# Performance work log

Hardware: AMD Instinct MI355X
Metric: run time of the kernel (lower is better)

Reference implementation:

```python
import jax, jax.numpy as jnp
import numpy as np

B, W, H, C = 8, 32, 32, 64   # batch, width, height, hidden_size
NH = 8                        # num_attention_heads
M = 32                        # max_position_embeddings
P = C // 2                    # position_embedding_size (query_positional_score=True)


def setup_inputs() -> dict:
    key = jax.random.key(0)
    ks = jax.random.split(key, 7)
    s = 0.02
    return {
        "hidden_states": jax.random.normal(ks[0], (B, W, H, C), dtype=jnp.float32),
        "row_emb": jax.random.normal(ks[1], (2 * M - 1, P), dtype=jnp.float32) * s,
        "col_emb": jax.random.normal(ks[2], (2 * M - 1, P), dtype=jnp.float32) * s,
        "Wq": jax.random.normal(ks[3], (NH * C, C), dtype=jnp.float32) * s,
        "bq": jnp.zeros((NH * C,), dtype=jnp.float32),
        "Wk": jax.random.normal(ks[4], (NH * C, C), dtype=jnp.float32) * s,
        "bk": jnp.zeros((NH * C,), dtype=jnp.float32),
        "Wv": jax.random.normal(ks[5], (C, NH * C), dtype=jnp.float32) * s,
        "bv": jnp.zeros((C,), dtype=jnp.float32),
    }


def reference(hidden_states, row_emb, col_emb, Wq, bq, Wk, bk, Wv, bv):
    b, w, h, c = hidden_states.shape
    nh = Wq.shape[0] // c
    half = c // 2
    center = row_emb.shape[0] // 2  # = max_position_embeddings - 1

    # projections: all_head_size = nh * c (per source: hidden_size * num_heads)
    q = (hidden_states @ Wq.T + bq).reshape(b, w, h, nh, c)
    k = (hidden_states @ Wk.T + bk).reshape(b, w, h, nh, c)

    # relative index tables: rel[i, j] = (j - i) + (M - 1)
    iw = jnp.arange(w)
    ih = jnp.arange(h)
    rel_w = iw[None, :] - iw[:, None] + center   # (w, w)
    rel_h = ih[None, :] - ih[:, None] + center   # (h, h)
    r_emb = row_emb[rel_w]  # (w, w, P)
    c_emb = col_emb[rel_h]  # (h, h, P)

    # positional scores: q split into row/col halves
    q_row = q[..., :half]
    q_col = q[..., half:]
    row_scores = jnp.einsum('bijhd,ikd->bijhk', q_row, r_emb)  # (b,w,h,nh,w)
    col_scores = jnp.einsum('bijhd,jld->bijhl', q_col, c_emb)  # (b,w,h,nh,h)
    scale = jnp.sqrt(jnp.asarray(c, dtype=hidden_states.dtype))
    scores = (row_scores[..., :, None] + col_scores[..., None, :]) / scale  # (b,w,h,nh,w,h)

    # content scores q^T k
    scores = scores + jnp.einsum('bijhd,bklhd->bijhkl', q, k) / scale

    # softmax over merged spatial key dims (k,l)
    probs = jax.nn.softmax(scores.reshape(b, w, h, nh, w * h), axis=-1).reshape(scores.shape)

    # value mixing directly with hidden_states, then output projection
    mixed = jnp.einsum('bijhkl,bkld->bijhd', probs, hidden_states).reshape(b, w, h, nh * c)
    return mixed @ Wv.T + bv
```

## Files before the change

kernel.cpp:

```cpp
#include <hip/hip_runtime.h>
#include <math.h>

typedef __bf16 bf16;
typedef bf16 bf16x2 __attribute__((ext_vector_type(2)));
typedef bf16 bf16x4 __attribute__((ext_vector_type(4)));
typedef bf16 bf16x8 __attribute__((ext_vector_type(8)));
typedef float f32x4 __attribute__((ext_vector_type(4)));

constexpr int CENTER = 31;

static __device__ __forceinline__ unsigned short f2bf_bits(float f) {
    bf16 b = (bf16)f;
    return __builtin_bit_cast(unsigned short, b);
}

__global__ __launch_bounds__(256)
void qkproj_kernel(const float* __restrict__ hid,
                   const float* __restrict__ Wq, const float* __restrict__ bq,
                   const float* __restrict__ Wk, const float* __restrict__ bk,
                   bf16* __restrict__ qb, bf16* __restrict__ kb,
                   bf16* __restrict__ htb)
{
    __shared__ __attribute__((aligned(16))) bf16 As[128][72];
    __shared__ __attribute__((aligned(16))) bf16 Bs[128][72];

    const int t  = threadIdx.x;
    const int pt = blockIdx.x;
    const int ot = blockIdx.y;
    const int z  = blockIdx.z;
    const float* W    = z ? Wk : Wq;
    const float* bias = z ? bk : bq;
    bf16* outp        = z ? kb : qb;
    const float scale = z ? 1.0f : 0.125f;
    const int p0 = pt * 128;
    const int b  = p0 >> 10;

    {
        int row = t >> 1, ch = (t & 1) * 32;
        const float4* asrc = (const float4*)(hid + (size_t)(p0 + row) * 64 + ch);
        const float4* bsrc = (const float4*)(W + (size_t)(ot * 128 + row) * 64 + ch);
        bf16 ta[32], tb[32];
        #pragma unroll
        for (int u = 0; u < 8; ++u) {
            float4 va = asrc[u], vb = bsrc[u];
            ta[4*u+0] = (bf16)va.x; ta[4*u+1] = (bf16)va.y;
            ta[4*u+2] = (bf16)va.z; ta[4*u+3] = (bf16)va.w;
            tb[4*u+0] = (bf16)vb.x; tb[4*u+1] = (bf16)vb.y;
            tb[4*u+2] = (bf16)vb.z; tb[4*u+3] = (bf16)vb.w;
        }
        #pragma unroll
        for (int u = 0; u < 4; ++u) {
            *(int4*)&As[row][ch + u * 8] = ((int4*)ta)[u];
            *(int4*)&Bs[row][ch + u * 8] = ((int4*)tb)[u];
        }
    }
    __syncthreads();

    if (ot == 0 && z == 0) {
        int d = t >> 2, ps = (t & 3) * 32;
        bf16* hdst = htb + ((size_t)b * 64 + d) * 1024 + (p0 & 1023) + ps;
        #pragma unroll
        for (int ii = 0; ii < 32; ii += 2) {
            ushort2 pk;
            pk.x = __builtin_bit_cast(unsigned short, As[ps + ii][d]);
            pk.y = __builtin_bit_cast(unsigned short, As[ps + ii + 1][d]);
            *(ushort2*)(hdst + ii) = pk;
        }
    }

    const int w = t >> 6, ln = t & 63, l15 = ln & 15, quad = ln >> 4;

    bf16x8 a[2][2];
    #pragma unroll
    for (int mt = 0; mt < 2; ++mt) {
        a[mt][0] = *(const bf16x8*)&As[w * 32 + mt * 16 + l15][quad * 8];
        a[mt][1] = *(const bf16x8*)&As[w * 32 + mt * 16 + l15][32 + quad * 8];
    }

    const f32x4 z4 = {0.f, 0.f, 0.f, 0.f};
    f32x4 acc[2][8];
    #pragma unroll
    for (int mt = 0; mt < 2; ++mt)
        #pragma unroll
        for (int nt = 0; nt < 8; ++nt) acc[mt][nt] = z4;

    #pragma unroll
    for (int nt = 0; nt < 8; ++nt) {
        bf16x8 b0 = *(const bf16x8*)&Bs[nt * 16 + l15][quad * 8];
        bf16x8 b1 = *(const bf16x8*)&Bs[nt * 16 + l15][32 + quad * 8];
        #pragma unroll
        for (int mt = 0; mt < 2; ++mt) {
            acc[mt][nt] = __builtin_amdgcn_mfma_f32_16x16x32_bf16(a[mt][0], b0, acc[mt][nt], 0, 0, 0);
            acc[mt][nt] = __builtin_amdgcn_mfma_f32_16x16x32_bf16(a[mt][1], b1, acc[mt][nt], 0, 0, 0);
        }
    }

    #pragma unroll
    for (int nt = 0; nt < 8; ++nt) {
        int o = ot * 128 + nt * 16 + l15;
        float bv = bias[o];
        int hh = o >> 6, d = o & 63;
        #pragma unroll
        for (int mt = 0; mt < 2; ++mt)
            #pragma unroll
            for (int r = 0; r < 4; ++r) {
                int pos = (p0 & 1023) + w * 32 + mt * 16 + quad * 4 + r;
                float val = (acc[mt][nt][r] + bv) * scale;
                outp[(((size_t)b * 8 + hh) * 1024 + pos) * 64 + d] = (bf16)val;
            }
    }
}

__global__ __launch_bounds__(256)
void bias_kernel(const bf16* __restrict__ qb,
                 const float* __restrict__ row_emb, const float* __restrict__ col_emb,
                 bf16* __restrict__ rowbias, bf16* __restrict__ colbias)
{
    __shared__ __attribute__((aligned(16))) bf16 embRs[63][40];
    __shared__ __attribute__((aligned(16))) bf16 embCs[63][40];

    const int t  = threadIdx.x;
    const int bh = blockIdx.x;
    const int sg = blockIdx.y;

    for (int i = t; i < 2016; i += 256) embRs[i >> 5][i & 31] = (bf16)row_emb[i];
    for (int i = t; i < 2016; i += 256) embCs[i >> 5][i & 31] = (bf16)col_emb[i];
    __syncthreads();

    const int w = t >> 6, ln = t & 63, l15 = ln & 15, quad = ln >> 4;

    #pragma unroll
    for (int u = 0; u < 4; ++u) {
        int s = sg * 16 + u * 4 + w;
        bool cm = s >= 32;
        int ij = cm ? s - 32 : s;

        bf16x8 a[2];
        #pragma unroll
        for (int mt = 0; mt < 2; ++mt) {
            const bf16* ap = cm
                ? qb + ((size_t)bh * 1024 + (mt * 16 + l15) * 32 + ij) * 64 + 32 + quad * 8
                : qb + ((size_t)bh * 1024 + ij * 32 + mt * 16 + l15) * 64 + quad * 8;
            a[mt] = *(const bf16x8*)ap;
        }
        bf16* ob = cm ? colbias : rowbias;

        #pragma unroll
        for (int nt = 0; nt < 2; ++nt) {
            int erow = nt * 16 + l15 + CENTER - ij;
            bf16x8 bfrag = cm ? *(const bf16x8*)&embCs[erow][quad * 8]
                              : *(const bf16x8*)&embRs[erow][quad * 8];
            #pragma unroll
            for (int mt = 0; mt < 2; ++mt) {
                f32x4 c = {0.f, 0.f, 0.f, 0.f};
                c = __builtin_amdgcn_mfma_f32_16x16x32_bf16(a[mt], bfrag, c, 0, 0, 0);
                #pragma unroll
                for (int r = 0; r < 4; ++r) {
                    int ql = mt * 16 + quad * 4 + r;
                    int qrow = cm ? ql * 32 + ij : ij * 32 + ql;
                    ob[((size_t)bh * 1024 + qrow) * 32 + nt * 16 + l15] = (bf16)c[r];
                }
            }
        }
    }
}

__global__ __launch_bounds__(256, 2)
void attn_kernel(const bf16* __restrict__ qb, const bf16* __restrict__ kb,
                 const bf16* __restrict__ htb,
                 const bf16* __restrict__ rowbias, const bf16* __restrict__ colbias,
                 bf16* __restrict__ mixedb)
{
    __shared__ __attribute__((aligned(16))) bf16 Ks[64][72];
    __shared__ __attribute__((aligned(16))) bf16 Hts[64][72];
    __shared__ __attribute__((aligned(16))) bf16 Pp[4][32][72];

    const int t  = threadIdx.x;
    const int qt = blockIdx.x;
    const int bh = blockIdx.y;
    const int b  = bh >> 3, h = bh & 7;
    const int q0 = qt * 128;
    const int w = t >> 6, ln = t & 63, l15 = ln & 15, quad = ln >> 4;

    bf16x8 bq_[2][2];
    float  cbv[2][2][4];
    const bf16* rbp[2];
    #pragma unroll
    for (int mt = 0; mt < 2; ++mt) {
        int qrow = q0 + w * 32 + mt * 16 + l15;
        const bf16* qp = qb + ((size_t)bh * 1024 + qrow) * 64;
        bq_[mt][0] = *(const bf16x8*)(qp + quad * 8);
        bq_[mt][1] = *(const bf16x8*)(qp + 32 + quad * 8);
        #pragma unroll
        for (int par = 0; par < 2; ++par) {
            bf16x4 cv = *(const bf16x4*)(colbias + ((size_t)bh * 1024 + qrow) * 32 + par * 16 + quad * 4);
            #pragma unroll
            for (int r = 0; r < 4; ++r) cbv[mt][par][r] = (float)cv[r];
        }
        rbp[mt] = rowbias + ((size_t)bh * 1024 + qrow) * 32;
    }

    const f32x4 z4 = {0.f, 0.f, 0.f, 0.f};
    f32x4 oacc[2][4];
    float lsum[2] = {0.f, 0.f};
    #pragma unroll
    for (int mt = 0; mt < 2; ++mt)
        #pragma unroll
        for (int dt = 0; dt < 4; ++dt) oacc[mt][dt] = z4;

    bf16* Pw = &Pp[w][0][0];
    const bf16* kcbase = kb + (size_t)bh * 1024 * 64;
    const bf16* hcbase = htb + (size_t)b * 64 * 1024;

    for (int kc = 0; kc < 16; ++kc) {
        __syncthreads();
        {
            int row = t >> 2, c = (t & 3) << 4;
            const bf16* ksrc = kcbase + (size_t)(kc * 64 + row) * 64 + c;
            *(int4*)&Ks[row][c]     = *(const int4*)ksrc;
            *(int4*)&Ks[row][c + 8] = *(const int4*)(ksrc + 8);
            const bf16* hsrc = hcbase + (size_t)row * 1024 + kc * 64 + c;
            *(int4*)&Hts[row][c]     = *(const int4*)hsrc;
            *(int4*)&Hts[row][c + 8] = *(const int4*)(hsrc + 8);
        }
        float rb[2][2];
        #pragma unroll
        for (int mt = 0; mt < 2; ++mt) {
            bf16x2 rv = *(const bf16x2*)(rbp[mt] + kc * 2);
            rb[mt][0] = (float)rv[0]; rb[mt][1] = (float)rv[1];
        }
        __syncthreads();

        f32x4 sf[2][4];
        #pragma unroll
        for (int mt = 0; mt < 2; ++mt)
            #pragma unroll
            for (int kt = 0; kt < 4; ++kt) sf[mt][kt] = z4;
        #pragma unroll
        for (int kt = 0; kt < 4; ++kt) {
            bf16x8 aK0 = *(const bf16x8*)&Ks[kt * 16 + l15][quad * 8];
            bf16x8 aK1 = *(const bf16x8*)&Ks[kt * 16 + l15][32 + quad * 8];
            #pragma unroll
            for (int mt = 0; mt < 2; ++mt) {
                sf[mt][kt] = __builtin_amdgcn_mfma_f32_16x16x32_bf16(aK0, bq_[mt][0], sf[mt][kt], 0, 0, 0);
                sf[mt][kt] = __builtin_amdgcn_mfma_f32_16x16x32_bf16(aK1, bq_[mt][1], sf[mt][kt], 0, 0, 0);
            }
        }

        #pragma unroll
        for (int mt = 0; mt < 2; ++mt)
            #pragma unroll
            for (int kt = 0; kt < 4; ++kt) {
                float rbv = rb[mt][kt >> 1];
                ushort4 pk;
                float p0 = __expf(sf[mt][kt][0] + rbv + cbv[mt][kt & 1][0]);
                float p1 = __expf(sf[mt][kt][1] + rbv + cbv[mt][kt & 1][1]);
                float p2 = __expf(sf[mt][kt][2] + rbv + cbv[mt][kt & 1][2]);
                float p3 = __expf(sf[mt][kt][3] + rbv + cbv[mt][kt & 1][3]);
                lsum[mt] += (p0 + p1) + (p2 + p3);
                pk.x = f2bf_bits(p0); pk.y = f2bf_bits(p1);
                pk.z = f2bf_bits(p2); pk.w = f2bf_bits(p3);
                *(ushort4*)&Pw[(mt * 16 + l15) * 72 + kt * 16 + quad * 4] = pk;
            }

        bf16x8 bp[2][2];
        #pragma unroll
        for (int mt = 0; mt < 2; ++mt) {
            bp[mt][0] = *(const bf16x8*)&Pw[(mt * 16 + l15) * 72 + quad * 8];
            bp[mt][1] = *(const bf16x8*)&Pw[(mt * 16 + l15) * 72 + 32 + quad * 8];
        }
        #pragma unroll
        for (int dt = 0; dt < 4; ++dt) {
            bf16x8 aH0 = *(const bf16x8*)&Hts[dt * 16 + l15][quad * 8];
            bf16x8 aH1 = *(const bf16x8*)&Hts[dt * 16 + l15][32 + quad * 8];
            #pragma unroll
            for (int mt = 0; mt < 2; ++mt) {
                oacc[mt][dt] = __builtin_amdgcn_mfma_f32_16x16x32_bf16(aH0, bp[mt][0], oacc[mt][dt], 0, 0, 0);
                oacc[mt][dt] = __builtin_amdgcn_mfma_f32_16x16x32_bf16(aH1, bp[mt][1], oacc[mt][dt], 0, 0, 0);
            }
        }
    }

    float inv[2];
    #pragma unroll
    for (int mt = 0; mt < 2; ++mt) {
        float v = lsum[mt];
        v += __shfl_xor(v, 16);
        v += __shfl_xor(v, 32);
        inv[mt] = 1.0f / v;
    }
    #pragma unroll
    for (int mt = 0; mt < 2; ++mt) {
        int pos = q0 + w * 32 + mt * 16 + l15;
        bf16* mb = mixedb + ((size_t)b * 1024 + pos) * 512 + h * 64;
        #pragma unroll
        for (int dt = 0; dt < 4; ++dt) {
            ushort4 pk;
            pk.x = f2bf_bits(oacc[mt][dt][0] * inv[mt]);
            pk.y = f2bf_bits(oacc[mt][dt][1] * inv[mt]);
            pk.z = f2bf_bits(oacc[mt][dt][2] * inv[mt]);
            pk.w = f2bf_bits(oacc[mt][dt][3] * inv[mt]);
            *(ushort4*)(mb + dt * 16 + quad * 4) = pk;
        }
    }
}

__global__ __launch_bounds__(256)
void out_proj_kernel(const bf16* __restrict__ mixedb,
                     const float* __restrict__ Wv, const float* __restrict__ bv,
                     float* __restrict__ out)
{
    __shared__ __attribute__((aligned(16))) bf16 Wvs[64][264];

    const int t  = threadIdx.x;
    const int p0 = blockIdx.x * 64;
    const int w = t >> 6, ln = t & 63, l15 = ln & 15, quad = ln >> 4;

    f32x4 acc[4];
    #pragma unroll
    for (int nt = 0; nt < 4; ++nt) {
        float bvv = bv[nt * 16 + l15];
        acc[nt] = (f32x4){bvv, bvv, bvv, bvv};
    }

    const bf16* arow = mixedb + (size_t)(p0 + w * 16 + l15) * 512;

    for (int half = 0; half < 2; ++half) {
        __syncthreads();
        {
            int c = t >> 2, seg = (t & 3) * 64;
            const float4* src = (const float4*)(Wv + (size_t)c * 512 + half * 256 + seg);
            #pragma unroll
            for (int u = 0; u < 16; ++u) {
                float4 v = src[u];
                bf16x4 pk = {(bf16)v.x, (bf16)v.y, (bf16)v.z, (bf16)v.w};
                *(bf16x4*)&Wvs[c][seg + u * 4] = pk;
            }
        }
        __syncthreads();

        #pragma unroll
        for (int kc = 0; kc < 8; ++kc) {
            bf16x8 a = *(const bf16x8*)(arow + half * 256 + kc * 32 + quad * 8);
            #pragma unroll
            for (int nt = 0; nt < 4; ++nt) {
                bf16x8 bfrag = *(const bf16x8*)&Wvs[nt * 16 + l15][kc * 32 + quad * 8];
                acc[nt] = __builtin_amdgcn_mfma_f32_16x16x32_bf16(a, bfrag, acc[nt], 0, 0, 0);
            }
        }
    }

    #pragma unroll
    for (int nt = 0; nt < 4; ++nt)
        #pragma unroll
        for (int r = 0; r < 4; ++r)
            out[(size_t)(p0 + w * 16 + quad * 4 + r) * 64 + nt * 16 + l15] = acc[nt][r];
}

extern "C" void kernel_launch(void* const* d_in, const int* in_sizes, int n_in,
                              void* d_out, int out_size, void* d_ws, size_t ws_size,
                              hipStream_t stream)
{
    const float* hid     = (const float*)d_in[0];
    const float* row_emb = (const float*)d_in[1];
    const float* col_emb = (const float*)d_in[2];
    const float* Wq      = (const float*)d_in[3];
    const float* bq      = (const float*)d_in[4];
    const float* Wk      = (const float*)d_in[5];
    const float* bk      = (const float*)d_in[6];
    const float* Wv      = (const float*)d_in[7];
    const float* bv      = (const float*)d_in[8];
    float* out = (float*)d_out;

    bf16* qb  = (bf16*)d_ws;
    bf16* kb  = qb + (size_t)64 * 1024 * 64;
    bf16* htb = kb + (size_t)64 * 1024 * 64;
    bf16* rowbias = htb + (size_t)8 * 64 * 1024;
    bf16* colbias = rowbias + (size_t)64 * 1024 * 32;
    bf16* mixedb  = colbias + (size_t)64 * 1024 * 32;

    qkproj_kernel<<<dim3(64, 4, 2), 256, 0, stream>>>(hid, Wq, bq, Wk, bk, qb, kb, htb);
    bias_kernel<<<dim3(64, 4), 256, 0, stream>>>(qb, row_emb, col_emb, rowbias, colbias);
    attn_kernel<<<dim3(8, 64), 256, 0, stream>>>(qb, kb, htb, rowbias, colbias, mixedb);
    out_proj_kernel<<<128, 256, 0, stream>>>(mixedb, Wv, bv, out);
}
```

Before: 135.1 us.

## Load K and hidden-state fragments directly from global in MFMA-ready layout

```diff
diff --git a/kernel.cpp b/kernel.cpp
--- a/kernel.cpp
+++ b/kernel.cpp
@@ -19,7 +19,7 @@
                    const float* __restrict__ Wq, const float* __restrict__ bq,
                    const float* __restrict__ Wk, const float* __restrict__ bk,
                    bf16* __restrict__ qb, bf16* __restrict__ kb,
-                   bf16* __restrict__ htb)
+                   bf16* __restrict__ htp)
 {
     __shared__ __attribute__((aligned(16))) bf16 As[128][72];
     __shared__ __attribute__((aligned(16))) bf16 Bs[128][72];
@@ -58,13 +58,18 @@
 
     if (ot == 0 && z == 0) {
         int d = t >> 2, ps = (t & 3) * 32;
-        bf16* hdst = htb + ((size_t)b * 64 + d) * 1024 + (p0 & 1023) + ps;
-        #pragma unroll
-        for (int ii = 0; ii < 32; ii += 2) {
-            ushort2 pk;
-            pk.x = __builtin_bit_cast(unsigned short, As[ps + ii][d]);
+        int pp = (p0 & 1023) + ps;
+        int kc = pp >> 6, half = (pp >> 5) & 1;
+        bf16* hdst = htp + (size_t)b * 65536 + kc * 4096 + half * 2048
+                         + (d >> 4) * 512 + (d & 15) * 32;
+        #pragma unroll
+        for (int ii = 0; ii < 32; ii += 4) {
+            ushort4 pk;
+            pk.x = __builtin_bit_cast(unsigned short, As[ps + ii + 0][d]);
             pk.y = __builtin_bit_cast(unsigned short, As[ps + ii + 1][d]);
-            *(ushort2*)(hdst + ii) = pk;
+            pk.z = __builtin_bit_cast(unsigned short, As[ps + ii + 2][d]);
+            pk.w = __builtin_bit_cast(unsigned short, As[ps + ii + 3][d]);
+            *(ushort4*)(hdst + ii) = pk;
         }
     }
 
@@ -165,14 +170,12 @@
     }
 }
 
-__global__ __launch_bounds__(256, 2)
+__global__ __launch_bounds__(256, 3)
 void attn_kernel(const bf16* __restrict__ qb, const bf16* __restrict__ kb,
-                 const bf16* __restrict__ htb,
+                 const bf16* __restrict__ htp,
                  const bf16* __restrict__ rowbias, const bf16* __restrict__ colbias,
                  bf16* __restrict__ mixedb)
 {
-    __shared__ __attribute__((aligned(16))) bf16 Ks[64][72];
-    __shared__ __attribute__((aligned(16))) bf16 Hts[64][72];
     __shared__ __attribute__((aligned(16))) bf16 Pp[4][32][72];
 
     const int t  = threadIdx.x;
@@ -209,42 +212,32 @@
         for (int dt = 0; dt < 4; ++dt) oacc[mt][dt] = z4;
 
     bf16* Pw = &Pp[w][0][0];
-    const bf16* kcbase = kb + (size_t)bh * 1024 * 64;
-    const bf16* hcbase = htb + (size_t)b * 64 * 1024;
+    const bf16* kfrag = kb + (size_t)bh * 65536 + (size_t)l15 * 64 + quad * 8;
+    const bf16* hfrag = htp + (size_t)b * 65536 + (size_t)l15 * 32 + quad * 8;
 
     for (int kc = 0; kc < 16; ++kc) {
-        __syncthreads();
-        {
-            int row = t >> 2, c = (t & 3) << 4;
-            const bf16* ksrc = kcbase + (size_t)(kc * 64 + row) * 64 + c;
-            *(int4*)&Ks[row][c]     = *(const int4*)ksrc;
-            *(int4*)&Ks[row][c + 8] = *(const int4*)(ksrc + 8);
-            const bf16* hsrc = hcbase + (size_t)row * 1024 + kc * 64 + c;
-            *(int4*)&Hts[row][c]     = *(const int4*)hsrc;
-            *(int4*)&Hts[row][c + 8] = *(const int4*)(hsrc + 8);
-        }
+        f32x4 sf[2][4];
+        #pragma unroll
+        for (int mt = 0; mt < 2; ++mt)
+            #pragma unroll
+            for (int kt = 0; kt < 4; ++kt) sf[mt][kt] = z4;
+        #pragma unroll
+        for (int kt = 0; kt < 4; ++kt) {
+            const bf16* kp = kfrag + (size_t)(kc * 64 + kt * 16) * 64;
+            bf16x8 aK0 = *(const bf16x8*)kp;
+            bf16x8 aK1 = *(const bf16x8*)(kp + 32);
+            #pragma unroll
+            for (int mt = 0; mt < 2; ++mt) {
+                sf[mt][kt] = __builtin_amdgcn_mfma_f32_16x16x32_bf16(aK0, bq_[mt][0], sf[mt][kt], 0, 0, 0);
+                sf[mt][kt] = __builtin_amdgcn_mfma_f32_16x16x32_bf16(aK1, bq_[mt][1], sf[mt][kt], 0, 0, 0);
+            }
+        }
+
         float rb[2][2];
         #pragma unroll
         for (int mt = 0; mt < 2; ++mt) {
             bf16x2 rv = *(const bf16x2*)(rbp[mt] + kc * 2);
             rb[mt][0] = (float)rv[0]; rb[mt][1] = (float)rv[1];
-        }
-        __syncthreads();
-
-        f32x4 sf[2][4];
-        #pragma unroll
-        for (int mt = 0; mt < 2; ++mt)
-            #pragma unroll
-            for (int kt = 0; kt < 4; ++kt) sf[mt][kt] = z4;
-        #pragma unroll
-        for (int kt = 0; kt < 4; ++kt) {
-            bf16x8 aK0 = *(const bf16x8*)&Ks[kt * 16 + l15][quad * 8];
-            bf16x8 aK1 = *(const bf16x8*)&Ks[kt * 16 + l15][32 + quad * 8];
-            #pragma unroll
-            for (int mt = 0; mt < 2; ++mt) {
-                sf[mt][kt] = __builtin_amdgcn_mfma_f32_16x16x32_bf16(aK0, bq_[mt][0], sf[mt][kt], 0, 0, 0);
-                sf[mt][kt] = __builtin_amdgcn_mfma_f32_16x16x32_bf16(aK1, bq_[mt][1], sf[mt][kt], 0, 0, 0);
-            }
         }
 
         #pragma unroll
@@ -271,8 +264,9 @@
         }
         #pragma unroll
         for (int dt = 0; dt < 4; ++dt) {
-            bf16x8 aH0 = *(const bf16x8*)&Hts[dt * 16 + l15][quad * 8];
-            bf16x8 aH1 = *(const bf16x8*)&Hts[dt * 16 + l15][32 + quad * 8];
+            const bf16* hp = hfrag + kc * 4096 + dt * 512;
+            bf16x8 aH0 = *(const bf16x8*)hp;
+            bf16x8 aH1 = *(const bf16x8*)(hp + 2048);
             #pragma unroll
             for (int mt = 0; mt < 2; ++mt) {
                 oacc[mt][dt] = __builtin_amdgcn_mfma_f32_16x16x32_bf16(aH0, bp[mt][0], oacc[mt][dt], 0, 0, 0);
@@ -374,13 +368,13 @@
 
     bf16* qb  = (bf16*)d_ws;
     bf16* kb  = qb + (size_t)64 * 1024 * 64;
-    bf16* htb = kb + (size_t)64 * 1024 * 64;
-    bf16* rowbias = htb + (size_t)8 * 64 * 1024;
+    bf16* htp = kb + (size_t)64 * 1024 * 64;
+    bf16* rowbias = htp + (size_t)8 * 64 * 1024;
     bf16* colbias = rowbias + (size_t)64 * 1024 * 32;
     bf16* mixedb  = colbias + (size_t)64 * 1024 * 32;
 
-    qkproj_kernel<<<dim3(64, 4, 2), 256, 0, stream>>>(hid, Wq, bq, Wk, bk, qb, kb, htb);
+    qkproj_kernel<<<dim3(64, 4, 2), 256, 0, stream>>>(hid, Wq, bq, Wk, bk, qb, kb, htp);
     bias_kernel<<<dim3(64, 4), 256, 0, stream>>>(qb, row_emb, col_emb, rowbias, colbias);
-    attn_kernel<<<dim3(8, 64), 256, 0, stream>>>(qb, kb, htb, rowbias, colbias, mixedb);
+    attn_kernel<<<dim3(8, 64), 256, 0, stream>>>(qb, kb, htp, rowbias, colbias, mixedb);
     out_proj_kernel<<<128, 256, 0, stream>>>(mixedb, Wv, bv, out);
 }
```

After: 157.3 us. 1.16x slower.

## Add prep kernel converting inputs and weights to bf16 once; merge Q/K projection blocks

Applied to the files above, without the earlier changes.

```diff
diff --git a/kernel.cpp b/kernel.cpp
--- a/kernel.cpp
+++ b/kernel.cpp
@@ -15,58 +15,94 @@
 }
 
 __global__ __launch_bounds__(256)
-void qkproj_kernel(const float* __restrict__ hid,
-                   const float* __restrict__ Wq, const float* __restrict__ bq,
-                   const float* __restrict__ Wk, const float* __restrict__ bk,
-                   bf16* __restrict__ qb, bf16* __restrict__ kb,
-                   bf16* __restrict__ htb)
+void prep_kernel(const float* __restrict__ hid,
+                 const float* __restrict__ Wq, const float* __restrict__ Wk,
+                 const float* __restrict__ Wv,
+                 bf16* __restrict__ hb, bf16* __restrict__ htb,
+                 bf16* __restrict__ Wqb, bf16* __restrict__ Wkb,
+                 bf16* __restrict__ Wvb)
+{
+    __shared__ __attribute__((aligned(16))) bf16 hs[64][72];
+
+    const int t   = threadIdx.x;
+    const int blk = blockIdx.x;
+    const int b   = blk >> 4, kc = blk & 15;
+
+    {
+        int row = t >> 2, c4 = (t & 3) * 16;
+        const float4* src = (const float4*)(hid + ((size_t)b * 1024 + kc * 64 + row) * 64 + c4);
+        bf16 tmp[16];
+        #pragma unroll
+        for (int u = 0; u < 4; ++u) {
+            float4 v = src[u];
+            tmp[4*u+0] = (bf16)v.x; tmp[4*u+1] = (bf16)v.y;
+            tmp[4*u+2] = (bf16)v.z; tmp[4*u+3] = (bf16)v.w;
+        }
+        *(int4*)&hs[row][c4]     = ((int4*)tmp)[0];
+        *(int4*)&hs[row][c4 + 8] = ((int4*)tmp)[1];
+        bf16* hdst = hb + ((size_t)b * 1024 + kc * 64 + row) * 64 + c4;
+        *(int4*)hdst       = ((int4*)tmp)[0];
+        *(int4*)(hdst + 8) = ((int4*)tmp)[1];
+    }
+
+    {
+        int idx = blk * 256 + t;
+        if (idx < 8192) {
+            float4 vq = ((const float4*)Wq)[idx];
+            float4 vk = ((const float4*)Wk)[idx];
+            float4 vv = ((const float4*)Wv)[idx];
+            ushort4 pq, pk2, pv;
+            pq.x = f2bf_bits(vq.x); pq.y = f2bf_bits(vq.y); pq.z = f2bf_bits(vq.z); pq.w = f2bf_bits(vq.w);
+            pk2.x = f2bf_bits(vk.x); pk2.y = f2bf_bits(vk.y); pk2.z = f2bf_bits(vk.z); pk2.w = f2bf_bits(vk.w);
+            pv.x = f2bf_bits(vv.x); pv.y = f2bf_bits(vv.y); pv.z = f2bf_bits(vv.z); pv.w = f2bf_bits(vv.w);
+            ((ushort4*)Wqb)[idx] = pq;
+            ((ushort4*)Wkb)[idx] = pk2;
+            ((ushort4*)Wvb)[idx] = pv;
+        }
+    }
+    __syncthreads();
+
+    {
+        int d = t >> 2, p0 = (t & 3) * 16;
+        ushort tmp[16];
+        #pragma unroll
+        for (int i = 0; i < 16; ++i)
+            tmp[i] = __builtin_bit_cast(unsigned short, hs[p0 + i][d]);
+        bf16* dst = htb + ((size_t)b * 64 + d) * 1024 + kc * 64 + p0;
+        *(int4*)dst       = ((int4*)tmp)[0];
+        *(int4*)(dst + 8) = ((int4*)tmp)[1];
+    }
+}
+
+__global__ __launch_bounds__(256)
+void qkproj_kernel(const bf16* __restrict__ hb,
+                   const bf16* __restrict__ Wqb, const float* __restrict__ bq,
+                   const bf16* __restrict__ Wkb, const float* __restrict__ bk,
+                   bf16* __restrict__ qb, bf16* __restrict__ kb)
 {
     __shared__ __attribute__((aligned(16))) bf16 As[128][72];
-    __shared__ __attribute__((aligned(16))) bf16 Bs[128][72];
+    __shared__ __attribute__((aligned(16))) bf16 Bqs[128][72];
+    __shared__ __attribute__((aligned(16))) bf16 Bks[128][72];
 
     const int t  = threadIdx.x;
     const int pt = blockIdx.x;
     const int ot = blockIdx.y;
-    const int z  = blockIdx.z;
-    const float* W    = z ? Wk : Wq;
-    const float* bias = z ? bk : bq;
-    bf16* outp        = z ? kb : qb;
-    const float scale = z ? 1.0f : 0.125f;
     const int p0 = pt * 128;
     const int b  = p0 >> 10;
 
     {
         int row = t >> 1, ch = (t & 1) * 32;
-        const float4* asrc = (const float4*)(hid + (size_t)(p0 + row) * 64 + ch);
-        const float4* bsrc = (const float4*)(W + (size_t)(ot * 128 + row) * 64 + ch);
-        bf16 ta[32], tb[32];
-        #pragma unroll
-        for (int u = 0; u < 8; ++u) {
-            float4 va = asrc[u], vb = bsrc[u];
-            ta[4*u+0] = (bf16)va.x; ta[4*u+1] = (bf16)va.y;
-            ta[4*u+2] = (bf16)va.z; ta[4*u+3] = (bf16)va.w;
-            tb[4*u+0] = (bf16)vb.x; tb[4*u+1] = (bf16)vb.y;
-            tb[4*u+2] = (bf16)vb.z; tb[4*u+3] = (bf16)vb.w;
-        }
+        const int4* asrc = (const int4*)(hb + (size_t)(p0 + row) * 64 + ch);
+        const int4* qsrc = (const int4*)(Wqb + (size_t)(ot * 128 + row) * 64 + ch);
+        const int4* ksrc = (const int4*)(Wkb + (size_t)(ot * 128 + row) * 64 + ch);
         #pragma unroll
         for (int u = 0; u < 4; ++u) {
-            *(int4*)&As[row][ch + u * 8] = ((int4*)ta)[u];
-            *(int4*)&Bs[row][ch + u * 8] = ((int4*)tb)[u];
+            *(int4*)&As[row][ch + u * 8]  = asrc[u];
+            *(int4*)&Bqs[row][ch + u * 8] = qsrc[u];
+            *(int4*)&Bks[row][ch + u * 8] = ksrc[u];
         }
     }
     __syncthreads();
-
-    if (ot == 0 && z == 0) {
-        int d = t >> 2, ps = (t & 3) * 32;
-        bf16* hdst = htb + ((size_t)b * 64 + d) * 1024 + (p0 & 1023) + ps;
-        #pragma unroll
-        for (int ii = 0; ii < 32; ii += 2) {
-            ushort2 pk;
-            pk.x = __builtin_bit_cast(unsigned short, As[ps + ii][d]);
-            pk.y = __builtin_bit_cast(unsigned short, As[ps + ii + 1][d]);
-            *(ushort2*)(hdst + ii) = pk;
-        }
-    }
 
     const int w = t >> 6, ln = t & 63, l15 = ln & 15, quad = ln >> 4;
 
@@ -78,36 +114,44 @@
     }
 
     const f32x4 z4 = {0.f, 0.f, 0.f, 0.f};
-    f32x4 acc[2][8];
-    #pragma unroll
-    for (int mt = 0; mt < 2; ++mt)
-        #pragma unroll
-        for (int nt = 0; nt < 8; ++nt) acc[mt][nt] = z4;
-
-    #pragma unroll
-    for (int nt = 0; nt < 8; ++nt) {
-        bf16x8 b0 = *(const bf16x8*)&Bs[nt * 16 + l15][quad * 8];
-        bf16x8 b1 = *(const bf16x8*)&Bs[nt * 16 + l15][32 + quad * 8];
-        #pragma unroll
-        for (int mt = 0; mt < 2; ++mt) {
-            acc[mt][nt] = __builtin_amdgcn_mfma_f32_16x16x32_bf16(a[mt][0], b0, acc[mt][nt], 0, 0, 0);
-            acc[mt][nt] = __builtin_amdgcn_mfma_f32_16x16x32_bf16(a[mt][1], b1, acc[mt][nt], 0, 0, 0);
-        }
-    }
-
-    #pragma unroll
-    for (int nt = 0; nt < 8; ++nt) {
-        int o = ot * 128 + nt * 16 + l15;
-        float bv = bias[o];
-        int hh = o >> 6, d = o & 63;
+
+    for (int z = 0; z < 2; ++z) {
+        const bf16 (* __restrict__ Bs)[72] = z ? Bks : Bqs;
+        const float* bias = z ? bk : bq;
+        bf16* outp        = z ? kb : qb;
+        const float scale = z ? 1.0f : 0.125f;
+
+        f32x4 acc[2][8];
         #pragma unroll
         for (int mt = 0; mt < 2; ++mt)
             #pragma unroll
-            for (int r = 0; r < 4; ++r) {
-                int pos = (p0 & 1023) + w * 32 + mt * 16 + quad * 4 + r;
-                float val = (acc[mt][nt][r] + bv) * scale;
-                outp[(((size_t)b * 8 + hh) * 1024 + pos) * 64 + d] = (bf16)val;
-            }
+            for (int nt = 0; nt < 8; ++nt) acc[mt][nt] = z4;
+
+        #pragma unroll
+        for (int nt = 0; nt < 8; ++nt) {
+            bf16x8 b0 = *(const bf16x8*)&Bs[nt * 16 + l15][quad * 8];
+            bf16x8 b1 = *(const bf16x8*)&Bs[nt * 16 + l15][32 + quad * 8];
+            #pragma unroll
+            for (int mt = 0; mt < 2; ++mt) {
+                acc[mt][nt] = __builtin_amdgcn_mfma_f32_16x16x32_bf16(a[mt][0], b0, acc[mt][nt], 0, 0, 0);
+                acc[mt][nt] = __builtin_amdgcn_mfma_f32_16x16x32_bf16(a[mt][1], b1, acc[mt][nt], 0, 0, 0);
+            }
+        }
+
+        #pragma unroll
+        for (int nt = 0; nt < 8; ++nt) {
+            int o = ot * 128 + nt * 16 + l15;
+            float bv = bias[o];
+            int hh = o >> 6, d = o & 63;
+            #pragma unroll
+            for (int mt = 0; mt < 2; ++mt)
+                #pragma unroll
+                for (int r = 0; r < 4; ++r) {
+                    int pos = (p0 & 1023) + w * 32 + mt * 16 + quad * 4 + r;
+                    float val = (acc[mt][nt][r] + bv) * scale;
+                    outp[(((size_t)b * 8 + hh) * 1024 + pos) * 64 + d] = (bf16)val;
+                }
+        }
     }
 }
 
@@ -307,7 +351,7 @@
 
 __global__ __launch_bounds__(256)
 void out_proj_kernel(const bf16* __restrict__ mixedb,
-                     const float* __restrict__ Wv, const float* __restrict__ bv,
+                     const bf16* __restrict__ Wvb, const float* __restrict__ bv,
                      float* __restrict__ out)
 {
     __shared__ __attribute__((aligned(16))) bf16 Wvs[64][264];
@@ -329,13 +373,10 @@
         __syncthreads();
         {
             int c = t >> 2, seg = (t & 3) * 64;
-            const float4* src = (const float4*)(Wv + (size_t)c * 512 + half * 256 + seg);
-            #pragma unroll
-            for (int u = 0; u < 16; ++u) {
-                float4 v = src[u];
-                bf16x4 pk = {(bf16)v.x, (bf16)v.y, (bf16)v.z, (bf16)v.w};
-                *(bf16x4*)&Wvs[c][seg + u * 4] = pk;
-            }
+            const int4* src = (const int4*)(Wvb + (size_t)c * 512 + half * 256 + seg);
+            #pragma unroll
+            for (int u = 0; u < 8; ++u)
+                *(int4*)&Wvs[c][seg + u * 8] = src[u];
         }
         __syncthreads();
 
@@ -372,15 +413,20 @@
     const float* bv      = (const float*)d_in[8];
     float* out = (float*)d_out;
 
-    bf16* qb  = (bf16*)d_ws;
-    bf16* kb  = qb + (size_t)64 * 1024 * 64;
-    bf16* htb = kb + (size_t)64 * 1024 * 64;
+    bf16* qb      = (bf16*)d_ws;
+    bf16* kb      = qb + (size_t)64 * 1024 * 64;
+    bf16* htb     = kb + (size_t)64 * 1024 * 64;
     bf16* rowbias = htb + (size_t)8 * 64 * 1024;
     bf16* colbias = rowbias + (size_t)64 * 1024 * 32;
     bf16* mixedb  = colbias + (size_t)64 * 1024 * 32;
-
-    qkproj_kernel<<<dim3(64, 4, 2), 256, 0, stream>>>(hid, Wq, bq, Wk, bk, qb, kb, htb);
+    bf16* hb      = mixedb + (size_t)8 * 1024 * 512;
+    bf16* Wqb     = hb + (size_t)8 * 1024 * 64;
+    bf16* Wkb     = Wqb + (size_t)512 * 64;
+    bf16* Wvb     = Wkb + (size_t)512 * 64;
+
+    prep_kernel<<<128, 256, 0, stream>>>(hid, Wq, Wk, Wv, hb, htb, Wqb, Wkb, Wvb);
+    qkproj_kernel<<<dim3(64, 4), 256, 0, stream>>>(hb, Wqb, bq, Wkb, bk, qb, kb);
     bias_kernel<<<dim3(64, 4), 256, 0, stream>>>(qb, row_emb, col_emb, rowbias, colbias);
     attn_kernel<<<dim3(8, 64), 256, 0, stream>>>(qb, kb, htb, rowbias, colbias, mixedb);
-    out_proj_kernel<<<128, 256, 0, stream>>>(mixedb, Wv, bv, out);
-}
+    out_proj_kernel<<<128, 256, 0, stream>>>(mixedb, Wvb, bv, out);
+}
```

New measurement: 131.5 us. 1.03x faster.
